# Kernel tuning notes

Measured on AMD Instinct MI355X. Metric: run time of the kernel, lower is better.

## Reference

```python
import jax, jax.numpy as jnp
import numpy as np

NUM_HEADS, NUM_KEYS, NUM_VALUES, NUM_OUTPUTS = 8, 64, 64, 512
B, H, W, C = 16, 64, 64, 512


def setup_inputs() -> dict:
    key = jax.random.key(0)
    ks = jax.random.split(key, 5)
    def xavier(k, shape):
        fan_in, fan_out = shape
        lim = np.sqrt(6.0 / (fan_in + fan_out))
        return jax.random.uniform(k, shape, jnp.float32, -lim, lim)
    return {
        "x": jax.random.normal(ks[0], (B, H, W, C), jnp.float32),
        "Wq": xavier(ks[1], (C, NUM_HEADS * NUM_KEYS)),
        "bq": jnp.zeros((NUM_HEADS * NUM_KEYS,), jnp.float32),
        "Wk": xavier(ks[2], (C, NUM_HEADS * NUM_KEYS)),
        "bk": jnp.zeros((NUM_HEADS * NUM_KEYS,), jnp.float32),
        "Wv": xavier(ks[3], (C, NUM_HEADS * NUM_VALUES)),
        "bv": jnp.zeros((NUM_HEADS * NUM_VALUES,), jnp.float32),
        "Wo": xavier(ks[4], (NUM_VALUES, NUM_OUTPUTS)),
        "bo": jnp.zeros((NUM_OUTPUTS,), jnp.float32),
    }


def reference(x, Wq, bq, Wk, bk, Wv, bv, Wo, bo):
    b, h, w, c = x.shape
    n, dk, dv = NUM_HEADS, NUM_KEYS, NUM_VALUES
    # single pooled query per image
    q = (jnp.mean(x, axis=(1, 2)) @ Wq + bq).reshape(b, n, dk)      # [B,N,dk]
    K = (x @ Wk + bk).reshape(b, h, w, n, dk)                        # [B,H,W,N,dk]
    V = (x @ Wv + bv).reshape(b, h, w, n, dv)                        # [B,H,W,N,dv]
    scale = 1.0 / jnp.sqrt(jnp.float32(dk))
    # scores of the single query against every pixel
    s = jnp.einsum('bnk,bhwnk->bnhw', q, K) * scale                  # [B,N,H,W]
    attn_h = jax.nn.softmax(s, axis=-1)   # per row, softmax over width
    attn_v = jax.nn.softmax(s, axis=-2)   # per column, softmax over height
    A_h = jnp.einsum('bnhw,bhwnv->bnhv', attn_h, V)                  # [B,N,H,dv]
    A_v = jnp.einsum('bnhw,bhwnv->bnwv', attn_v, V)                  # [B,N,W,dv]
    # outer-product combine over spatial dims, summed over heads
    A = jnp.einsum('bnhv,bnwv->bhwv', A_h, A_v)                      # [B,H,W,dv]
    return A @ Wo + bo                                               # [B,H,W,num_outputs]
```

## Files before the change

### kernel.cpp

```cpp
#include <hip/hip_runtime.h>
#include <hip/hip_bf16.h>

#define NHEADS 8
#define DK 64
#define DV 64
#define CIN 512
#define PIX_PER_IMG 4096
#define NPIX 65536

typedef short bf16x8 __attribute__((ext_vector_type(8)));
typedef float f32x4 __attribute__((ext_vector_type(4)));

__device__ __forceinline__ float b2f(unsigned int u) {
  union { unsigned int i; float f; } v; v.i = u << 16; return v.f;
}
__device__ __forceinline__ unsigned short f2b(float f) {
  union { float f; unsigned int i; } v; v.f = f;
  unsigned int x = v.i;
  return (unsigned short)((x + 0x7fffu + ((x >> 16) & 1u)) >> 16);
}
__device__ __forceinline__ void gload_lds16(const void* g, void* l) {
  __builtin_amdgcn_global_load_lds(
      (const __attribute__((address_space(1))) void*)g,
      (__attribute__((address_space(3))) void*)l, 16, 0, 0);
}

__global__ void k_pool_convert(const float* __restrict__ x,
                               unsigned short* __restrict__ xb,
                               float* __restrict__ partial) {
  int blk = blockIdx.x;
  int b = blk >> 6, chunk = blk & 63;
  int t = threadIdx.x;
  size_t base = ((size_t)b * PIX_PER_IMG + (size_t)chunk * 64) * CIN;
  const float* xp = x + base;
  unsigned short* xbp = xb + base;
  float a0 = 0.f, a1 = 0.f;
  for (int p = 0; p < 64; ++p) {
    float v0 = xp[p * CIN + t];
    float v1 = xp[p * CIN + t + 256];
    a0 += v0; a1 += v1;
    xbp[p * CIN + t] = f2b(v0);
    xbp[p * CIN + t + 256] = f2b(v1);
  }
  partial[(size_t)blk * CIN + t] = a0;
  partial[(size_t)blk * CIN + t + 256] = a1;
}

__global__ void k_xbar(const float* __restrict__ partial, float* __restrict__ xbar) {
  int gid = blockIdx.x * 256 + threadIdx.x;
  int b = gid >> 9, c = gid & 511;
  float s = 0.f;
  for (int ch = 0; ch < 64; ++ch) s += partial[((size_t)(b * 64 + ch)) * CIN + c];
  xbar[gid] = s * (1.0f / 4096.0f);
}

__global__ void k_q(const float* __restrict__ xbar,
                    const float* __restrict__ Wq, const float* __restrict__ bq,
                    const float* __restrict__ bk,
                    float* __restrict__ qbuf, float* __restrict__ s0) {
  __shared__ float xs[CIN];
  __shared__ float red[256];
  __shared__ float qs[64];
  int b = blockIdx.x, n = blockIdx.y, t = threadIdx.x;
  xs[t] = xbar[b * CIN + t];
  xs[t + 256] = xbar[b * CIN + t + 256];
  __syncthreads();
  int jj = t & 63, part = t >> 6;
  float acc = 0.f;
  const float* wp = Wq + (size_t)(part * 128) * CIN + n * 64 + jj;
  for (int ci = 0; ci < 128; ++ci)
    acc += xs[part * 128 + ci] * wp[(size_t)ci * CIN];
  red[t] = acc;
  __syncthreads();
  if (t < 64) {
    float q = red[t] + red[t + 64] + red[t + 128] + red[t + 192] + bq[n * 64 + t];
    qbuf[b * CIN + n * 64 + t] = q;
    qs[t] = q * bk[n * 64 + t];
  }
  __syncthreads();
  if (t == 0) {
    float s = 0.f;
    for (int k = 0; k < 64; ++k) s += qs[k];
    s0[b * NHEADS + n] = s;
  }
}

__global__ void k_p(const float* __restrict__ qbuf, const float* __restrict__ Wk,
                    float* __restrict__ P) {
  __shared__ float wks[64 * 65];
  __shared__ float qs2[16 * 64];
  int n = blockIdx.x, cchunk = blockIdx.y, t = threadIdx.x;
  int c0 = cchunk * 64;
  for (int i = 0; i < 4; ++i) {
    int idx = i * 256 + t;
    int bb = idx >> 6, k = idx & 63;
    qs2[idx] = qbuf[bb * CIN + n * 64 + k];
  }
  int k = t & 63;
  for (int i = 0; i < 16; ++i) {
    int r = i * 4 + (t >> 6);
    wks[k * 65 + r] = Wk[(size_t)(c0 + r) * CIN + n * 64 + k];
  }
  __syncthreads();
  int c = t & 63, bg = t >> 6;
  for (int b2 = bg * 4; b2 < bg * 4 + 4; ++b2) {
    float acc = 0.f;
    for (int kk = 0; kk < 64; ++kk) acc += qs2[b2 * 64 + kk] * wks[kk * 65 + c];
    P[((size_t)(b2 * NHEADS + n)) * CIN + c0 + c] = acc;
  }
}

__global__ void k_prep_w(const float* __restrict__ Wv, const float* __restrict__ Wo,
                         unsigned short* __restrict__ WvT, unsigned short* __restrict__ WoT) {
  int idx = blockIdx.x * 256 + threadIdx.x;
  if (idx < 262144) {
    int n = idx >> 9, c = idx & 511;
    WvT[idx] = f2b(Wv[(size_t)c * 512 + n]);
  } else {
    int j = idx - 262144;
    int o = j >> 6, kk = j & 63;
    WoT[j] = f2b(Wo[(size_t)kk * 512 + o]);
  }
}

template <int KTILES, bool OUT_BF16>
__global__ void k_gemm(const unsigned short* __restrict__ A,
                       const unsigned short* __restrict__ BT,
                       const float* __restrict__ bias,
                       void* __restrict__ Cout) {
  __shared__ __align__(16) unsigned short As[128 * 64];
  __shared__ __align__(16) unsigned short Bs[128 * 64];
  const int t = threadIdx.x;
  const int wave = t >> 6, lane = t & 63;
  const int wr = wave >> 1, wc = wave & 1;
  const int m0 = blockIdx.y * 128, n0 = blockIdx.x * 128;
  const int K = KTILES * 64;

  f32x4 acc[4][4];
  for (int i = 0; i < 4; ++i)
    for (int j = 0; j < 4; ++j) acc[i][j] = (f32x4){0.f, 0.f, 0.f, 0.f};

  const int srow = wave * 32 + (lane >> 3);
  const int scolb = (lane & 7) * 16;

  for (int kt = 0; kt < KTILES; ++kt) {
    __syncthreads();
    const char* gA = (const char*)A + ((size_t)(m0 + srow) * K + kt * 64) * 2 + scolb;
    const char* gB = (const char*)BT + ((size_t)(n0 + srow) * K + kt * 64) * 2 + scolb;
    char* lA = (char*)As + wave * 4096;
    char* lB = (char*)Bs + wave * 4096;
#pragma unroll
    for (int j = 0; j < 4; ++j) {
      gload_lds16(gA + (size_t)j * 8 * K * 2, lA + j * 1024);
      gload_lds16(gB + (size_t)j * 8 * K * 2, lB + j * 1024);
    }
    __syncthreads();
#pragma unroll
    for (int s = 0; s < 2; ++s) {
      bf16x8 af[4], bg[4];
#pragma unroll
      for (int i = 0; i < 4; ++i) {
        int mrow = wr * 64 + i * 16 + (lane & 15);
        af[i] = *(const bf16x8*)((const char*)As + mrow * 128 + s * 64 + ((lane >> 4) * 16));
      }
#pragma unroll
      for (int j = 0; j < 4; ++j) {
        int nrow = wc * 64 + j * 16 + (lane & 15);
        bg[j] = *(const bf16x8*)((const char*)Bs + nrow * 128 + s * 64 + ((lane >> 4) * 16));
      }
#pragma unroll
      for (int i = 0; i < 4; ++i)
#pragma unroll
        for (int j = 0; j < 4; ++j)
          acc[i][j] = __builtin_amdgcn_mfma_f32_16x16x32_bf16(af[i], bg[j], acc[i][j], 0, 0, 0);
    }
  }
#pragma unroll
  for (int i = 0; i < 4; ++i)
#pragma unroll
    for (int j = 0; j < 4; ++j) {
      int mbase = m0 + wr * 64 + i * 16 + ((lane >> 4) * 4);
      int n = n0 + wc * 64 + j * 16 + (lane & 15);
      float bb = bias[n];
#pragma unroll
      for (int r = 0; r < 4; ++r) {
        float v = acc[i][j][r] + bb;
        if (OUT_BF16)
          ((unsigned short*)Cout)[(size_t)(mbase + r) * 512 + n] = f2b(v);
        else
          ((float*)Cout)[(size_t)(mbase + r) * 512 + n] = v;
      }
    }
}

__global__ void k_scores(const unsigned short* __restrict__ xb,
                         const float* __restrict__ P, const float* __restrict__ s0,
                         float* __restrict__ s) {
  __shared__ float Pl[NHEADS * 516];
  __shared__ float s0l[NHEADS];
  int blk = blockIdx.x;
  int b = blk >> 7, tile = blk & 127;
  int t = threadIdx.x;
  for (int idx = t; idx < NHEADS * CIN; idx += 256) {
    int n = idx >> 9, c = idx & 511;
    Pl[n * 516 + c] = P[((size_t)(b * NHEADS + n)) * CIN + c];
  }
  if (t < NHEADS) s0l[t] = s0[b * NHEADS + t];
  __syncthreads();
  int pl = t >> 3, n = t & 7;
  int pix = tile * 32 + pl;
  const uint4* xr = (const uint4*)(xb + ((size_t)b * PIX_PER_IMG + pix) * CIN);
  const float* Pr = Pl + n * 516;
  float acc = s0l[n];
  for (int cc = 0; cc < 64; ++cc) {
    uint4 u = xr[cc];
    int c = cc * 8;
    acc += b2f(u.x & 0xffff) * Pr[c + 0];
    acc += b2f(u.x >> 16) * Pr[c + 1];
    acc += b2f(u.y & 0xffff) * Pr[c + 2];
    acc += b2f(u.y >> 16) * Pr[c + 3];
    acc += b2f(u.z & 0xffff) * Pr[c + 4];
    acc += b2f(u.z >> 16) * Pr[c + 5];
    acc += b2f(u.w & 0xffff) * Pr[c + 6];
    acc += b2f(u.w >> 16) * Pr[c + 7];
  }
  s[((size_t)(b * NHEADS + n)) * PIX_PER_IMG + pix] = acc * 0.125f;
}

__global__ void k_softmax(const float* __restrict__ s,
                          float* __restrict__ ah, float* __restrict__ avT) {
  __shared__ float st[4096];
  int bn = blockIdx.x, t = threadIdx.x;
  const float* sp = s + (size_t)bn * 4096;
  for (int i = t; i < 4096; i += 256) st[i] = sp[i];
  __syncthreads();
  if (t < 64) {
    int h = t;
    float m = -1e30f;
    for (int w = 0; w < 64; ++w) m = fmaxf(m, st[h * 64 + w]);
    float sum = 0.f;
    for (int w = 0; w < 64; ++w) sum += __expf(st[h * 64 + w] - m);
    float inv = 1.f / sum;
    for (int w = 0; w < 64; ++w)
      ah[(size_t)bn * 4096 + h * 64 + w] = __expf(st[h * 64 + w] - m) * inv;
  } else if (t < 128) {
    int w = t - 64;
    float m = -1e30f;
    for (int h = 0; h < 64; ++h) m = fmaxf(m, st[h * 64 + w]);
    float sum = 0.f;
    for (int h = 0; h < 64; ++h) sum += __expf(st[h * 64 + w] - m);
    float inv = 1.f / sum;
    for (int h = 0; h < 64; ++h)
      avT[(size_t)bn * 4096 + w * 64 + h] = __expf(st[h * 64 + w] - m) * inv;
  }
}

__global__ void k_xh(const unsigned short* __restrict__ xb,
                     const float* __restrict__ ahg,
                     unsigned short* __restrict__ XHV) {
  __shared__ unsigned short xs[64 * 256];
  __shared__ float ahl[NHEADS * 64];
  int bh = blockIdx.x, ch = blockIdx.y, t = threadIdx.x;
  int b = bh >> 6, h = bh & 63;
  const unsigned short* src = xb + ((size_t)(b * PIX_PER_IMG + h * 64)) * CIN + ch * 256;
#pragma unroll
  for (int i = 0; i < 8; ++i) {
    int idx = i * 256 + t;
    int w = idx >> 5, off = idx & 31;
    ((uint4*)xs)[idx] = ((const uint4*)(src + (size_t)w * CIN))[off];
  }
#pragma unroll
  for (int i = 0; i < 2; ++i) {
    int idx = i * 256 + t;
    ahl[idx] = ahg[((size_t)(b * NHEADS + (idx >> 6))) * PIX_PER_IMG + h * 64 + (idx & 63)];
  }
  __syncthreads();
  int n = t >> 5, oct = t & 31;
  float acc[8] = {0.f, 0.f, 0.f, 0.f, 0.f, 0.f, 0.f, 0.f};
  const float* ar = ahl + n * 64;
  for (int w = 0; w < 64; ++w) {
    float aw = ar[w];
    uint4 u = *(const uint4*)(xs + (size_t)w * 256 + oct * 8);
    acc[0] += aw * b2f(u.x & 0xffff);
    acc[1] += aw * b2f(u.x >> 16);
    acc[2] += aw * b2f(u.y & 0xffff);
    acc[3] += aw * b2f(u.y >> 16);
    acc[4] += aw * b2f(u.z & 0xffff);
    acc[5] += aw * b2f(u.z >> 16);
    acc[6] += aw * b2f(u.w & 0xffff);
    acc[7] += aw * b2f(u.w >> 16);
  }
  uint4 o;
  o.x = (unsigned)f2b(acc[0]) | ((unsigned)f2b(acc[1]) << 16);
  o.y = (unsigned)f2b(acc[2]) | ((unsigned)f2b(acc[3]) << 16);
  o.z = (unsigned)f2b(acc[4]) | ((unsigned)f2b(acc[5]) << 16);
  o.w = (unsigned)f2b(acc[6]) | ((unsigned)f2b(acc[7]) << 16);
  size_t dst = ((size_t)(n * 2048 + b * 64 + h)) * CIN + ch * 256 + oct * 8;
  *(uint4*)(XHV + dst) = o;
}

__global__ void k_xv(const unsigned short* __restrict__ xb,
                     const float* __restrict__ avTg,
                     unsigned short* __restrict__ XHV) {
  __shared__ unsigned short xs[64 * 256];
  __shared__ float avl[NHEADS * 64];
  int bw = blockIdx.x, ch = blockIdx.y, t = threadIdx.x;
  int b = bw >> 6, w = bw & 63;
#pragma unroll
  for (int i = 0; i < 8; ++i) {
    int idx = i * 256 + t;
    int h = idx >> 5, off = idx & 31;
    ((uint4*)xs)[idx] =
        ((const uint4*)(xb + ((size_t)(b * PIX_PER_IMG + h * 64 + w)) * CIN + ch * 256))[off];
  }
#pragma unroll
  for (int i = 0; i < 2; ++i) {
    int idx = i * 256 + t;
    avl[idx] = avTg[((size_t)(b * NHEADS + (idx >> 6))) * PIX_PER_IMG + w * 64 + (idx & 63)];
  }
  __syncthreads();
  int n = t >> 5, oct = t & 31;
  float acc[8] = {0.f, 0.f, 0.f, 0.f, 0.f, 0.f, 0.f, 0.f};
  const float* ar = avl + n * 64;
  for (int h = 0; h < 64; ++h) {
    float aw = ar[h];
    uint4 u = *(const uint4*)(xs + (size_t)h * 256 + oct * 8);
    acc[0] += aw * b2f(u.x & 0xffff);
    acc[1] += aw * b2f(u.x >> 16);
    acc[2] += aw * b2f(u.y & 0xffff);
    acc[3] += aw * b2f(u.y >> 16);
    acc[4] += aw * b2f(u.z & 0xffff);
    acc[5] += aw * b2f(u.z >> 16);
    acc[6] += aw * b2f(u.w & 0xffff);
    acc[7] += aw * b2f(u.w >> 16);
  }
  uint4 o;
  o.x = (unsigned)f2b(acc[0]) | ((unsigned)f2b(acc[1]) << 16);
  o.y = (unsigned)f2b(acc[2]) | ((unsigned)f2b(acc[3]) << 16);
  o.z = (unsigned)f2b(acc[4]) | ((unsigned)f2b(acc[5]) << 16);
  o.w = (unsigned)f2b(acc[6]) | ((unsigned)f2b(acc[7]) << 16);
  size_t dst = ((size_t)(n * 2048 + 1024 + b * 64 + w)) * CIN + ch * 256 + oct * 8;
  *(uint4*)(XHV + dst) = o;
}

__global__ void k_gemm2(const unsigned short* __restrict__ XHV,
                        const unsigned short* __restrict__ WvT,
                        const float* __restrict__ bv,
                        float* __restrict__ Ah, float* __restrict__ Av) {
  __shared__ __align__(16) unsigned short As[128 * 64];
  __shared__ __align__(16) unsigned short Bs[64 * 64];
  const int t = threadIdx.x;
  const int wave = t >> 6, lane = t & 63;
  const int mtile = blockIdx.x, head = blockIdx.y;
  const int m0 = mtile * 128;
  const unsigned short* A = XHV + (size_t)head * 2048 * CIN;
  const unsigned short* BT = WvT + (size_t)head * 64 * CIN;

  f32x4 acc[2][4];
  for (int i = 0; i < 2; ++i)
    for (int j = 0; j < 4; ++j) acc[i][j] = (f32x4){0.f, 0.f, 0.f, 0.f};

  const int lrow = wave * 8 + (lane >> 3);
  const int lcolb = (lane & 7) * 16;

  for (int kt = 0; kt < 8; ++kt) {
    __syncthreads();
#pragma unroll
    for (int j = 0; j < 4; ++j) {
      gload_lds16((const char*)A + ((size_t)(m0 + j * 32 + lrow) * CIN + kt * 64) * 2 + lcolb,
                  (char*)As + (j * 32 + wave * 8) * 128);
    }
#pragma unroll
    for (int j = 0; j < 2; ++j) {
      gload_lds16((const char*)BT + ((size_t)(j * 32 + lrow) * CIN + kt * 64) * 2 + lcolb,
                  (char*)Bs + (j * 32 + wave * 8) * 128);
    }
    __syncthreads();
#pragma unroll
    for (int s = 0; s < 2; ++s) {
      bf16x8 af[2], bg[4];
#pragma unroll
      for (int i = 0; i < 2; ++i) {
        int mrow = wave * 32 + i * 16 + (lane & 15);
        af[i] = *(const bf16x8*)((const char*)As + mrow * 128 + s * 64 + ((lane >> 4) * 16));
      }
#pragma unroll
      for (int j = 0; j < 4; ++j) {
        int nrow = j * 16 + (lane & 15);
        bg[j] = *(const bf16x8*)((const char*)Bs + nrow * 128 + s * 64 + ((lane >> 4) * 16));
      }
#pragma unroll
      for (int i = 0; i < 2; ++i)
#pragma unroll
        for (int j = 0; j < 4; ++j)
          acc[i][j] = __builtin_amdgcn_mfma_f32_16x16x32_bf16(af[i], bg[j], acc[i][j], 0, 0, 0);
    }
  }
#pragma unroll
  for (int i = 0; i < 2; ++i)
#pragma unroll
    for (int j = 0; j < 4; ++j) {
      int v = j * 16 + (lane & 15);
      float bb = bv[head * 64 + v];
#pragma unroll
      for (int r = 0; r < 4; ++r) {
        int m = m0 + wave * 32 + i * 16 + ((lane >> 4) * 4) + r;
        float val = acc[i][j][r] + bb;
        if (m < 1024) {
          int b = m >> 6, h = m & 63;
          Ah[((size_t)(b * NHEADS + head)) * 4096 + h * 64 + v] = val;
        } else {
          int m2 = m - 1024;
          int b = m2 >> 6, w = m2 & 63;
          Av[((size_t)(b * NHEADS + head)) * 4096 + w * 64 + v] = val;
        }
      }
    }
}

__global__ void k_combine(const float* __restrict__ Ah, const float* __restrict__ Av,
                          unsigned short* __restrict__ Af) {
  int t = threadIdx.x;
  int g = blockIdx.x * 4 + (t >> 6);
  int v = t & 63;
  int b = g >> 12;
  int rem = g & 4095;
  int h = rem >> 6, w = rem & 63;
  float a = 0.f;
#pragma unroll
  for (int n = 0; n < 8; ++n) {
    int bn = b * 8 + n;
    a += Ah[((size_t)bn * 64 + h) * 64 + v] * Av[((size_t)bn * 64 + w) * 64 + v];
  }
  Af[(size_t)g * 64 + v] = f2b(a);
}

extern "C" void kernel_launch(void* const* d_in, const int* in_sizes, int n_in,
                              void* d_out, int out_size, void* d_ws, size_t ws_size,
                              hipStream_t stream) {
  (void)in_sizes; (void)n_in; (void)out_size; (void)ws_size;
  const float* x = (const float*)d_in[0];
  const float* Wq = (const float*)d_in[1];
  const float* bq = (const float*)d_in[2];
  const float* Wk = (const float*)d_in[3];
  const float* bk = (const float*)d_in[4];
  const float* Wv = (const float*)d_in[5];
  const float* bv = (const float*)d_in[6];
  const float* Wo = (const float*)d_in[7];
  const float* bo = (const float*)d_in[8];
  float* out = (float*)d_out;

  char* ws = (char*)d_ws;
  unsigned short* xb = (unsigned short*)(ws + 0);
  float* s = (float*)(ws + 67108864);
  float* partial = (float*)(ws + 75497472);
  float* xbar = (float*)(ws + 77594624);
  float* qbuf = (float*)(ws + 77627392);
  float* P = (float*)(ws + 77660160);
  float* s0 = (float*)(ws + 77922304);
  float* attn_h = (float*)(ws + 77922816);
  float* avT = (float*)(ws + 80019968);
  unsigned short* XHV = (unsigned short*)(ws + 82117120);
  float* Ah = (float*)(ws + 98894336);
  float* Av = (float*)(ws + 100991488);
  unsigned short* Af = (unsigned short*)(ws + 103088640);
  unsigned short* WvT = (unsigned short*)(ws + 111477248);
  unsigned short* WoT = (unsigned short*)(ws + 112001536);

  k_pool_convert<<<1024, 256, 0, stream>>>(x, xb, partial);
  k_xbar<<<32, 256, 0, stream>>>(partial, xbar);
  k_q<<<dim3(16, 8), 256, 0, stream>>>(xbar, Wq, bq, bk, qbuf, s0);
  k_p<<<dim3(8, 8), 256, 0, stream>>>(qbuf, Wk, P);
  k_prep_w<<<1152, 256, 0, stream>>>(Wv, Wo, WvT, WoT);
  k_scores<<<2048, 256, 0, stream>>>(xb, P, s0, s);
  k_softmax<<<128, 256, 0, stream>>>(s, attn_h, avT);
  k_xh<<<dim3(1024, 2), 256, 0, stream>>>(xb, attn_h, XHV);
  k_xv<<<dim3(1024, 2), 256, 0, stream>>>(xb, avT, XHV);
  k_gemm2<<<dim3(16, 8), 256, 0, stream>>>(XHV, WvT, bv, Ah, Av);
  k_combine<<<16384, 256, 0, stream>>>(Ah, Av, Af);
  k_gemm<1, false><<<dim3(4, 512), 256, 0, stream>>>(Af, WoT, bo, (void*)out);
}
```

Baseline: 375.9 us.

## Fuse combine into output GEMM, merge q/P kernels, vectorize pooling

Folds the head-summed outer-product combine directly into the output GEMM's LDS tile fill, which removes the bf16 Af intermediate (16M elements) and one launch. Merges the xbar reduction, the q projection and the P=q·Wk^T computation into a single small kernel. Vectorizes the pool/convert kernel to float4 loads with packed bf16 stores. The trade-off is that the combine is recomputed inside each of the 4 N-tile blocks, and the q/P work now runs on only 128 blocks.

```diff
diff --git a/kernel.cpp b/kernel.cpp
--- a/kernel.cpp
+++ b/kernel.cpp
@@ -31,82 +31,60 @@
   int blk = blockIdx.x;
   int b = blk >> 6, chunk = blk & 63;
   int t = threadIdx.x;
-  size_t base = ((size_t)b * PIX_PER_IMG + (size_t)chunk * 64) * CIN;
-  const float* xp = x + base;
-  unsigned short* xbp = xb + base;
-  float a0 = 0.f, a1 = 0.f;
-  for (int p = 0; p < 64; ++p) {
-    float v0 = xp[p * CIN + t];
-    float v1 = xp[p * CIN + t + 256];
-    a0 += v0; a1 += v1;
-    xbp[p * CIN + t] = f2b(v0);
-    xbp[p * CIN + t + 256] = f2b(v1);
-  }
-  partial[(size_t)blk * CIN + t] = a0;
-  partial[(size_t)blk * CIN + t + 256] = a1;
-}
-
-__global__ void k_xbar(const float* __restrict__ partial, float* __restrict__ xbar) {
-  int gid = blockIdx.x * 256 + threadIdx.x;
-  int b = gid >> 9, c = gid & 511;
-  float s = 0.f;
-  for (int ch = 0; ch < 64; ++ch) s += partial[((size_t)(b * 64 + ch)) * CIN + c];
-  xbar[gid] = s * (1.0f / 4096.0f);
-}
-
-__global__ void k_q(const float* __restrict__ xbar,
-                    const float* __restrict__ Wq, const float* __restrict__ bq,
-                    const float* __restrict__ bk,
-                    float* __restrict__ qbuf, float* __restrict__ s0) {
+  int c4 = t & 127;
+  int half = t >> 7;
+  size_t rowbase = (size_t)b * PIX_PER_IMG + chunk * 64;
+  const float4* x4 = (const float4*)x;
+  float4 acc = make_float4(0.f, 0.f, 0.f, 0.f);
+#pragma unroll 4
+  for (int i = 0; i < 32; ++i) {
+    int p = 2 * i + half;
+    float4 v = x4[(rowbase + p) * 128 + c4];
+    acc.x += v.x; acc.y += v.y; acc.z += v.z; acc.w += v.w;
+    uint2 o;
+    o.x = (unsigned)f2b(v.x) | ((unsigned)f2b(v.y) << 16);
+    o.y = (unsigned)f2b(v.z) | ((unsigned)f2b(v.w) << 16);
+    *(uint2*)(xb + (rowbase + p) * CIN + c4 * 4) = o;
+  }
+  *(float4*)(partial + ((size_t)(blk * 2 + half)) * CIN + c4 * 4) = acc;
+}
+
+__global__ void k_qp2(const float* __restrict__ partial,
+                      const float* __restrict__ Wq, const float* __restrict__ bq,
+                      const float* __restrict__ Wk, const float* __restrict__ bk,
+                      float* __restrict__ P, float* __restrict__ s0) {
   __shared__ float xs[CIN];
   __shared__ float red[256];
-  __shared__ float qs[64];
+  __shared__ float qsh[64];
   int b = blockIdx.x, n = blockIdx.y, t = threadIdx.x;
-  xs[t] = xbar[b * CIN + t];
-  xs[t + 256] = xbar[b * CIN + t + 256];
+  for (int c = t; c < CIN; c += 256) {
+    float s = 0.f;
+    for (int ch = 0; ch < 128; ++ch) s += partial[((size_t)(b * 128 + ch)) * CIN + c];
+    xs[c] = s * (1.0f / 4096.0f);
+  }
   __syncthreads();
   int jj = t & 63, part = t >> 6;
-  float acc = 0.f;
-  const float* wp = Wq + (size_t)(part * 128) * CIN + n * 64 + jj;
-  for (int ci = 0; ci < 128; ++ci)
-    acc += xs[part * 128 + ci] * wp[(size_t)ci * CIN];
-  red[t] = acc;
-  __syncthreads();
-  if (t < 64) {
-    float q = red[t] + red[t + 64] + red[t + 128] + red[t + 192] + bq[n * 64 + t];
-    qbuf[b * CIN + n * 64 + t] = q;
-    qs[t] = q * bk[n * 64 + t];
-  }
+  {
+    float acc = 0.f;
+    const float* wp = Wq + (size_t)(part * 128) * CIN + n * 64 + jj;
+    for (int ci = 0; ci < 128; ++ci)
+      acc += xs[part * 128 + ci] * wp[(size_t)ci * CIN];
+    red[t] = acc;
+  }
+  __syncthreads();
+  if (t < 64)
+    qsh[t] = red[t] + red[t + 64] + red[t + 128] + red[t + 192] + bq[n * 64 + t];
   __syncthreads();
   if (t == 0) {
     float s = 0.f;
-    for (int k = 0; k < 64; ++k) s += qs[k];
+    for (int k = 0; k < 64; ++k) s += qsh[k] * bk[n * 64 + k];
     s0[b * NHEADS + n] = s;
   }
-}
-
-__global__ void k_p(const float* __restrict__ qbuf, const float* __restrict__ Wk,
-                    float* __restrict__ P) {
-  __shared__ float wks[64 * 65];
-  __shared__ float qs2[16 * 64];
-  int n = blockIdx.x, cchunk = blockIdx.y, t = threadIdx.x;
-  int c0 = cchunk * 64;
-  for (int i = 0; i < 4; ++i) {
-    int idx = i * 256 + t;
-    int bb = idx >> 6, k = idx & 63;
-    qs2[idx] = qbuf[bb * CIN + n * 64 + k];
-  }
-  int k = t & 63;
-  for (int i = 0; i < 16; ++i) {
-    int r = i * 4 + (t >> 6);
-    wks[k * 65 + r] = Wk[(size_t)(c0 + r) * CIN + n * 64 + k];
-  }
-  __syncthreads();
-  int c = t & 63, bg = t >> 6;
-  for (int b2 = bg * 4; b2 < bg * 4 + 4; ++b2) {
+  for (int c = t; c < CIN; c += 256) {
     float acc = 0.f;
-    for (int kk = 0; kk < 64; ++kk) acc += qs2[b2 * 64 + kk] * wks[kk * 65 + c];
-    P[((size_t)(b2 * NHEADS + n)) * CIN + c0 + c] = acc;
+    const float* wr = Wk + (size_t)c * CIN + n * 64;
+    for (int k = 0; k < 64; ++k) acc += qsh[k] * wr[k];
+    P[((size_t)(b * NHEADS + n)) * CIN + c] = acc;
   }
 }
 
@@ -121,76 +99,6 @@
     int o = j >> 6, kk = j & 63;
     WoT[j] = f2b(Wo[(size_t)kk * 512 + o]);
   }
-}
-
-template <int KTILES, bool OUT_BF16>
-__global__ void k_gemm(const unsigned short* __restrict__ A,
-                       const unsigned short* __restrict__ BT,
-                       const float* __restrict__ bias,
-                       void* __restrict__ Cout) {
-  __shared__ __align__(16) unsigned short As[128 * 64];
-  __shared__ __align__(16) unsigned short Bs[128 * 64];
-  const int t = threadIdx.x;
-  const int wave = t >> 6, lane = t & 63;
-  const int wr = wave >> 1, wc = wave & 1;
-  const int m0 = blockIdx.y * 128, n0 = blockIdx.x * 128;
-  const int K = KTILES * 64;
-
-  f32x4 acc[4][4];
-  for (int i = 0; i < 4; ++i)
-    for (int j = 0; j < 4; ++j) acc[i][j] = (f32x4){0.f, 0.f, 0.f, 0.f};
-
-  const int srow = wave * 32 + (lane >> 3);
-  const int scolb = (lane & 7) * 16;
-
-  for (int kt = 0; kt < KTILES; ++kt) {
-    __syncthreads();
-    const char* gA = (const char*)A + ((size_t)(m0 + srow) * K + kt * 64) * 2 + scolb;
-    const char* gB = (const char*)BT + ((size_t)(n0 + srow) * K + kt * 64) * 2 + scolb;
-    char* lA = (char*)As + wave * 4096;
-    char* lB = (char*)Bs + wave * 4096;
-#pragma unroll
-    for (int j = 0; j < 4; ++j) {
-      gload_lds16(gA + (size_t)j * 8 * K * 2, lA + j * 1024);
-      gload_lds16(gB + (size_t)j * 8 * K * 2, lB + j * 1024);
-    }
-    __syncthreads();
-#pragma unroll
-    for (int s = 0; s < 2; ++s) {
-      bf16x8 af[4], bg[4];
-#pragma unroll
-      for (int i = 0; i < 4; ++i) {
-        int mrow = wr * 64 + i * 16 + (lane & 15);
-        af[i] = *(const bf16x8*)((const char*)As + mrow * 128 + s * 64 + ((lane >> 4) * 16));
-      }
-#pragma unroll
-      for (int j = 0; j < 4; ++j) {
-        int nrow = wc * 64 + j * 16 + (lane & 15);
-        bg[j] = *(const bf16x8*)((const char*)Bs + nrow * 128 + s * 64 + ((lane >> 4) * 16));
-      }
-#pragma unroll
-      for (int i = 0; i < 4; ++i)
-#pragma unroll
-        for (int j = 0; j < 4; ++j)
-          acc[i][j] = __builtin_amdgcn_mfma_f32_16x16x32_bf16(af[i], bg[j], acc[i][j], 0, 0, 0);
-    }
-  }
-#pragma unroll
-  for (int i = 0; i < 4; ++i)
-#pragma unroll
-    for (int j = 0; j < 4; ++j) {
-      int mbase = m0 + wr * 64 + i * 16 + ((lane >> 4) * 4);
-      int n = n0 + wc * 64 + j * 16 + (lane & 15);
-      float bb = bias[n];
-#pragma unroll
-      for (int r = 0; r < 4; ++r) {
-        float v = acc[i][j][r] + bb;
-        if (OUT_BF16)
-          ((unsigned short*)Cout)[(size_t)(mbase + r) * 512 + n] = f2b(v);
-        else
-          ((float*)Cout)[(size_t)(mbase + r) * 512 + n] = v;
-      }
-    }
 }
 
 __global__ void k_scores(const unsigned short* __restrict__ xb,
@@ -418,21 +326,80 @@
     }
 }
 
-__global__ void k_combine(const float* __restrict__ Ah, const float* __restrict__ Av,
-                          unsigned short* __restrict__ Af) {
-  int t = threadIdx.x;
-  int g = blockIdx.x * 4 + (t >> 6);
-  int v = t & 63;
-  int b = g >> 12;
-  int rem = g & 4095;
-  int h = rem >> 6, w = rem & 63;
-  float a = 0.f;
-#pragma unroll
-  for (int n = 0; n < 8; ++n) {
-    int bn = b * 8 + n;
-    a += Ah[((size_t)bn * 64 + h) * 64 + v] * Av[((size_t)bn * 64 + w) * 64 + v];
-  }
-  Af[(size_t)g * 64 + v] = f2b(a);
+__global__ void k_outgemm(const float* __restrict__ Ah, const float* __restrict__ Av,
+                          const unsigned short* __restrict__ WoT,
+                          const float* __restrict__ bo, float* __restrict__ out) {
+  __shared__ __align__(16) unsigned short As[128 * 64];
+  __shared__ __align__(16) unsigned short Bs[128 * 64];
+  const int t = threadIdx.x;
+  const int wave = t >> 6, lane = t & 63;
+  const int wr = wave >> 1, wc = wave & 1;
+  const int m0 = blockIdx.y * 128, n0 = blockIdx.x * 128;
+  const int b = m0 >> 12, h0 = (m0 >> 6) & 63;
+
+  const int srow = wave * 32 + (lane >> 3), scolb = (lane & 7) * 16;
+#pragma unroll
+  for (int j = 0; j < 4; ++j)
+    gload_lds16((const char*)WoT + ((size_t)(n0 + srow + j * 8) * 64) * 2 + scolb,
+                (char*)Bs + wave * 4096 + j * 1024);
+
+  {
+    const int v = t & 63, rg = t >> 6;
+    float ahv0[8], ahv1[8];
+#pragma unroll
+    for (int n = 0; n < 8; ++n) {
+      ahv0[n] = Ah[((size_t)((b * 8 + n) * 64 + h0)) * 64 + v];
+      ahv1[n] = Ah[((size_t)((b * 8 + n) * 64 + h0 + 1)) * 64 + v];
+    }
+#pragma unroll 2
+    for (int i = 0; i < 16; ++i) {
+      int w = rg * 16 + i;
+      float a0 = 0.f, a1 = 0.f;
+#pragma unroll
+      for (int n = 0; n < 8; ++n) {
+        float av = Av[((size_t)((b * 8 + n) * 64 + w)) * 64 + v];
+        a0 += ahv0[n] * av;
+        a1 += ahv1[n] * av;
+      }
+      As[w * 64 + v] = f2b(a0);
+      As[(64 + w) * 64 + v] = f2b(a1);
+    }
+  }
+  __syncthreads();
+
+  f32x4 acc[4][4];
+  for (int i = 0; i < 4; ++i)
+    for (int j = 0; j < 4; ++j) acc[i][j] = (f32x4){0.f, 0.f, 0.f, 0.f};
+#pragma unroll
+  for (int s = 0; s < 2; ++s) {
+    bf16x8 af[4], bg[4];
+#pragma unroll
+    for (int i = 0; i < 4; ++i) {
+      int mrow = wr * 64 + i * 16 + (lane & 15);
+      af[i] = *(const bf16x8*)((const char*)As + mrow * 128 + s * 64 + ((lane >> 4) * 16));
+    }
+#pragma unroll
+    for (int j = 0; j < 4; ++j) {
+      int nrow = wc * 64 + j * 16 + (lane & 15);
+      bg[j] = *(const bf16x8*)((const char*)Bs + nrow * 128 + s * 64 + ((lane >> 4) * 16));
+    }
+#pragma unroll
+    for (int i = 0; i < 4; ++i)
+#pragma unroll
+      for (int j = 0; j < 4; ++j)
+        acc[i][j] = __builtin_amdgcn_mfma_f32_16x16x32_bf16(af[i], bg[j], acc[i][j], 0, 0, 0);
+  }
+#pragma unroll
+  for (int i = 0; i < 4; ++i)
+#pragma unroll
+    for (int j = 0; j < 4; ++j) {
+      int mbase = m0 + wr * 64 + i * 16 + ((lane >> 4) * 4);
+      int n = n0 + wc * 64 + j * 16 + (lane & 15);
+      float bb = bo[n];
+#pragma unroll
+      for (int r = 0; r < 4; ++r)
+        out[(size_t)(mbase + r) * 512 + n] = acc[i][j][r] + bb;
+    }
 }
 
 extern "C" void kernel_launch(void* const* d_in, const int* in_sizes, int n_in,
@@ -453,30 +420,24 @@
   char* ws = (char*)d_ws;
   unsigned short* xb = (unsigned short*)(ws + 0);
   float* s = (float*)(ws + 67108864);
-  float* partial = (float*)(ws + 75497472);
-  float* xbar = (float*)(ws + 77594624);
-  float* qbuf = (float*)(ws + 77627392);
-  float* P = (float*)(ws + 77660160);
-  float* s0 = (float*)(ws + 77922304);
-  float* attn_h = (float*)(ws + 77922816);
-  float* avT = (float*)(ws + 80019968);
-  unsigned short* XHV = (unsigned short*)(ws + 82117120);
-  float* Ah = (float*)(ws + 98894336);
-  float* Av = (float*)(ws + 100991488);
-  unsigned short* Af = (unsigned short*)(ws + 103088640);
-  unsigned short* WvT = (unsigned short*)(ws + 111477248);
-  unsigned short* WoT = (unsigned short*)(ws + 112001536);
+  float* partial = (float*)(ws + 69206016);
+  float* P = (float*)(ws + 73400320);
+  float* s0 = (float*)(ws + 73662464);
+  float* attn_h = (float*)(ws + 73662976);
+  float* avT = (float*)(ws + 75760128);
+  unsigned short* XHV = (unsigned short*)(ws + 77857280);
+  float* Ah = (float*)(ws + 94634496);
+  float* Av = (float*)(ws + 96731648);
+  unsigned short* WvT = (unsigned short*)(ws + 98828800);
+  unsigned short* WoT = (unsigned short*)(ws + 99353088);
 
   k_pool_convert<<<1024, 256, 0, stream>>>(x, xb, partial);
-  k_xbar<<<32, 256, 0, stream>>>(partial, xbar);
-  k_q<<<dim3(16, 8), 256, 0, stream>>>(xbar, Wq, bq, bk, qbuf, s0);
-  k_p<<<dim3(8, 8), 256, 0, stream>>>(qbuf, Wk, P);
+  k_qp2<<<dim3(16, 8), 256, 0, stream>>>(partial, Wq, bq, Wk, bk, P, s0);
   k_prep_w<<<1152, 256, 0, stream>>>(Wv, Wo, WvT, WoT);
   k_scores<<<2048, 256, 0, stream>>>(xb, P, s0, s);
   k_softmax<<<128, 256, 0, stream>>>(s, attn_h, avT);
   k_xh<<<dim3(1024, 2), 256, 0, stream>>>(xb, attn_h, XHV);
   k_xv<<<dim3(1024, 2), 256, 0, stream>>>(xb, avT, XHV);
   k_gemm2<<<dim3(16, 8), 256, 0, stream>>>(XHV, WvT, bv, Ah, Av);
-  k_combine<<<16384, 256, 0, stream>>>(Ah, Av, Af);
-  k_gemm<1, false><<<dim3(4, 512), 256, 0, stream>>>(Af, WoT, bo, (void*)out);
-}
+  k_outgemm<<<dim3(4, 512), 256, 0, stream>>>(Ah, Av, WoT, bo, out);
+}
```

After: 371.7 us. Within noise of the previous version (-1.1%).
